# Kernel tuning notes

Measured on AMD Instinct MI355X. Metric: run time of the kernel, lower is better.

The kernel has to match this reference:

```python
import jax, jax.numpy as jnp
import numpy as np

B, T, D, H, DFF = 2, 2048, 1024, 16, 4096
K = D // H  # head size = 64
EPS = 1e-5


def _layernorm(x, g, b):
    mu = jnp.mean(x, axis=-1, keepdims=True)
    var = jnp.mean(jnp.square(x - mu), axis=-1, keepdims=True)
    return (x - mu) * jax.lax.rsqrt(var + EPS) * g + b


def setup_inputs() -> dict:
    key = jax.random.key(0)
    ks = jax.random.split(key, 12)
    s_attn = 1.0 / np.sqrt(D)
    s_ff1 = 1.0 / np.sqrt(D)
    s_ff2 = 1.0 / np.sqrt(DFF)
    return {
        "x": jax.random.normal(ks[0], (B, T, D), jnp.float32),
        # per-head q/k/v projections, stacked: [H, D, K] (each head's Linear has no bias)
        "Wq": jax.random.normal(ks[1], (H, D, K), jnp.float32) * s_attn,
        "Wk": jax.random.normal(ks[2], (H, D, K), jnp.float32) * s_attn,
        "Wv": jax.random.normal(ks[3], (H, D, K), jnp.float32) * s_attn,
        "Wo": jax.random.normal(ks[4], (D, D), jnp.float32) * s_attn,
        "bo": jax.random.normal(ks[5], (D,), jnp.float32) * 0.01,
        "W1": jax.random.normal(ks[6], (D, DFF), jnp.float32) * s_ff1,
        "b1": jax.random.normal(ks[7], (DFF,), jnp.float32) * 0.01,
        "W2": jax.random.normal(ks[8], (DFF, D), jnp.float32) * s_ff2,
        "b2": jax.random.normal(ks[9], (D,), jnp.float32) * 0.01,
        "g1": jnp.ones((D,), jnp.float32),
        "be1": jnp.zeros((D,), jnp.float32),
        "g2": jnp.ones((D,), jnp.float32),
        "be2": jnp.zeros((D,), jnp.float32),
    }


def reference(x, Wq, Wk, Wv, Wo, bo, W1, b1, W2, b2, g1, be1, g2, be2):
    b, t, d = x.shape
    h = _layernorm(x, g1, be1)
    # multi-head attention (per-head linear projections, fused via einsum)
    q = jnp.einsum('btd,hdk->bhtk', h, Wq)
    k = jnp.einsum('btd,hdk->bhtk', h, Wk)
    v = jnp.einsum('btd,hdk->bhtk', h, Wv)
    scores = jnp.einsum('bhtk,bhsk->bhts', q, k) * (K ** -0.5)
    causal = jnp.tril(jnp.ones((t, t), bool))
    scores = jnp.where(causal, scores, -jnp.inf)
    attn = jax.nn.softmax(scores, axis=-1)
    o = jnp.einsum('bhts,bhsk->bhtk', attn, v)
    o = o.transpose(0, 2, 1, 3).reshape(b, t, d)  # concat heads
    x = x + o @ Wo + bo
    # feed-forward (exact GELU, as torch default)
    h2 = _layernorm(x, g2, be2)
    ff = jax.nn.gelu(h2 @ W1 + b1, approximate=False) @ W2 + b2
    return x + ff
```

## Files before the change

kernel.cpp:

```cpp
#include <hip/hip_runtime.h>
#include <hip/hip_bf16.h>


#define BT   4096
#define DIM  1024
#define DFF  4096
#define TSEQ 2048
#define NHEAD 16
#define HDIM 64
#define QKV_LD 3072

typedef __attribute__((ext_vector_type(8))) short  bf16x8;
typedef __attribute__((ext_vector_type(4))) float  floatx4;

__device__ __forceinline__ void async_copy16(const __hip_bfloat16* g, __hip_bfloat16* l) {
    __builtin_amdgcn_global_load_lds(
        (const __attribute__((address_space(1))) void*)g,
        (__attribute__((address_space(3))) void*)l, 16, 0, 0);
}

__device__ __forceinline__ floatx4 mfma_bf16(bf16x8 a, bf16x8 b, floatx4 c) {
    return __builtin_amdgcn_mfma_f32_16x16x32_bf16(a, b, c, 0, 0, 0);
}

__device__ __forceinline__ void ln_body(const float* __restrict__ x,
                                        const float* __restrict__ g,
                                        const float* __restrict__ be,
                                        __hip_bfloat16* __restrict__ out,
                                        int row, float* red) {
    const int t = threadIdx.x;
    const float4 v = ((const float4*)(x + (size_t)row * DIM))[t];
    float s  = v.x + v.y + v.z + v.w;
    float ss = v.x * v.x + v.y * v.y + v.z * v.z + v.w * v.w;
    for (int d = 1; d < 64; d <<= 1) { s += __shfl_xor(s, d); ss += __shfl_xor(ss, d); }
    const int w = t >> 6;
    if ((t & 63) == 0) { red[w] = s; red[w + 4] = ss; }
    __syncthreads();
    s  = red[0] + red[1] + red[2] + red[3];
    ss = red[4] + red[5] + red[6] + red[7];
    const float mu = s * (1.0f / DIM);
    const float rstd = rsqrtf(ss * (1.0f / DIM) - mu * mu + 1e-5f);
    const float4 gv = ((const float4*)g)[t];
    const float4 bv = ((const float4*)be)[t];
    __hip_bfloat16* o = out + (size_t)row * DIM + t * 4;
    o[0] = __float2bfloat16((v.x - mu) * rstd * gv.x + bv.x);
    o[1] = __float2bfloat16((v.y - mu) * rstd * gv.y + bv.y);
    o[2] = __float2bfloat16((v.z - mu) * rstd * gv.z + bv.z);
    o[3] = __float2bfloat16((v.w - mu) * rstd * gv.w + bv.w);
}

__global__ __launch_bounds__(256) void ln_kernel(const float* __restrict__ x,
                                                 const float* __restrict__ g,
                                                 const float* __restrict__ be,
                                                 __hip_bfloat16* __restrict__ out) {
    __shared__ float red[8];
    ln_body(x, g, be, out, blockIdx.x, red);
}

__device__ __forceinline__ void tc_body(const float* __restrict__ src, int src_ld,
                                        __hip_bfloat16* __restrict__ dst, int dst_ld,
                                        int bx, int by, float* tile ) {
    const int r0 = bx * 64, c0 = by * 64;
    const int tr = threadIdx.x >> 6;
    const int tc = threadIdx.x & 63;
    for (int i = 0; i < 16; ++i) {
        const int r = i * 4 + tr;
        tile[r * 65 + tc] = src[(size_t)(r0 + r) * src_ld + c0 + tc];
    }
    __syncthreads();
    for (int i = 0; i < 16; ++i) {
        const int c = i * 4 + tr;
        dst[(size_t)(c0 + c) * dst_ld + r0 + tc] = __float2bfloat16(tile[tc * 65 + c]);
    }
}

__global__ __launch_bounds__(256) void prep_kernel(const float* __restrict__ x,
                                                   const float* __restrict__ g1,
                                                   const float* __restrict__ be1,
                                                   const float* __restrict__ Wq,
                                                   const float* __restrict__ Wk,
                                                   const float* __restrict__ Wv,
                                                   const float* __restrict__ Wo,
                                                   const float* __restrict__ W1,
                                                   const float* __restrict__ W2,
                                                   __hip_bfloat16* __restrict__ h1,
                                                   __hip_bfloat16* __restrict__ WqkvT,
                                                   __hip_bfloat16* __restrict__ WoT,
                                                   __hip_bfloat16* __restrict__ W1T,
                                                   __hip_bfloat16* __restrict__ W2T) {
    __shared__ __align__(16) float smemf[64 * 65];
    const int id = blockIdx.x;
    if (id < 4096) {
        ln_body(x, g1, be1, h1, id, smemf);
    } else if (id < 4096 + 768) {
        const int i = id - 4096;
        const int bx = i & 15, hz = i >> 4;
        const int proj = hz >> 4, h = hz & 15;
        const float* W = (proj == 0 ? Wq : (proj == 1 ? Wk : Wv)) + (size_t)h * DIM * HDIM;
        const int r0 = bx * 64;
        const int tr = threadIdx.x >> 6, tc = threadIdx.x & 63;
        for (int i2 = 0; i2 < 16; ++i2) {
            const int r = i2 * 4 + tr;
            smemf[r * 65 + tc] = W[(size_t)(r0 + r) * HDIM + tc];
        }
        __syncthreads();
        for (int i2 = 0; i2 < 16; ++i2) {
            const int k = i2 * 4 + tr;
            WqkvT[(size_t)(proj * 1024 + h * 64 + k) * DIM + r0 + tc] =
                __float2bfloat16(smemf[tc * 65 + k]);
        }
    } else if (id < 4096 + 768 + 256) {
        const int i = id - (4096 + 768);
        tc_body(Wo, 1024, WoT, 1024, i & 15, i >> 4, smemf);
    } else if (id < 4096 + 768 + 256 + 1024) {
        const int i = id - (4096 + 768 + 256);
        tc_body(W1, 4096, W1T, 1024, i & 15, i >> 4, smemf);
    } else {
        const int i = id - (4096 + 768 + 256 + 1024);
        tc_body(W2, 1024, W2T, 4096, i & 63, i >> 6, smemf);
    }
}

__global__ __launch_bounds__(256) void transpose_v(const __hip_bfloat16* __restrict__ qkv,
                                                   __hip_bfloat16* __restrict__ vt) {
    __shared__ __align__(16) __hip_bfloat16 tile[64 * 72];
    const int t = threadIdx.x;
    const int bh = blockIdx.y;
    const int b = bh >> 4, h = bh & 15;
    const int t0 = blockIdx.x * 64;
    const __hip_bfloat16* src = qkv + (size_t)b * TSEQ * QKV_LD + 2048 + h * HDIM;
    const int lo = t >> 3, k8 = t & 7;
    for (int i = 0; i < 2; ++i) {
        const int rr = i * 32 + lo;
        const bf16x8 v = *(const bf16x8*)(src + (size_t)(t0 + rr) * QKV_LD + k8 * 8);
        const int cb = k8 ^ ((rr >> 3) & 7);
        *(bf16x8*)(tile + rr * 72 + cb * 8) = v;
    }
    __syncthreads();
    for (int i = 0; i < 2; ++i) {
        const int dd = i * 32 + lo;
        const int c0 = dd >> 3, cl = dd & 7;
        bf16x8 o;
        for (int jj = 0; jj < 8; ++jj) {
            const int key = k8 * 8 + jj;
            o[jj] = *(const short*)(tile + key * 72 + (c0 ^ ((key >> 3) & 7)) * 8 + cl);
        }
        *(bf16x8*)(vt + ((size_t)bh * HDIM + dd) * TSEQ + t0 + k8 * 8) = o;
    }
}

template <int EPI>
__global__ __launch_bounds__(256) void gemm_bt(const __hip_bfloat16* __restrict__ A,
                                               const __hip_bfloat16* __restrict__ Bt,
                                               __hip_bfloat16* __restrict__ outb,
                                               const float* __restrict__ bias,
                                               int M, int N, int K) {
    __shared__ __align__(16) __hip_bfloat16 As[4][128 * 32];
    __shared__ __align__(16) __hip_bfloat16 Bs[4][128 * 32];
    const int t = threadIdx.x;
    const int w = t >> 6, l = t & 63;
    const int quad = l >> 4, tl = l & 15;
    const int wr = w >> 1, wc = w & 1;
    const int m0 = blockIdx.y * 128, n0 = blockIdx.x * 128;

    floatx4 acc[4][4] = {};
    const int rowA = t >> 2;
    const int c8 = (t & 3) << 3;

    for (int k0 = 0; k0 < K; k0 += 128) {
        __syncthreads();
        for (int sub = 0; sub < 4; ++sub) {
            const int kk = k0 + sub * 32;
            const __hip_bfloat16* gA = A + (size_t)(m0 + rowA) * K + kk + c8;
            const __hip_bfloat16* gB = Bt + (size_t)(n0 + rowA) * K + kk + c8;
            async_copy16(gA,                  As[sub] + w * 512);
            async_copy16(gA + (size_t)64 * K, As[sub] + 2048 + w * 512);
            async_copy16(gB,                  Bs[sub] + w * 512);
            async_copy16(gB + (size_t)64 * K, Bs[sub] + 2048 + w * 512);
        }
        __syncthreads();

        for (int ks = 0; ks < 4; ++ks) {
            bf16x8 af[4], bfr[4];
            const int aRow = wr * 64 + tl;
            const int bRow = wc * 64 + tl;
            for (int mi = 0; mi < 4; ++mi)
                af[mi] = *(const bf16x8*)(As[ks] + (aRow + mi * 16) * 32 + quad * 8);
            for (int ni = 0; ni < 4; ++ni)
                bfr[ni] = *(const bf16x8*)(Bs[ks] + (bRow + ni * 16) * 32 + quad * 8);
            for (int mi = 0; mi < 4; ++mi)
                for (int ni = 0; ni < 4; ++ni)
                    acc[mi][ni] = mfma_bf16(af[mi], bfr[ni], acc[mi][ni]);
        }
    }

    const int rowBase = m0 + wr * 64 + quad * 4;
    const int colBase = n0 + wc * 64 + tl;
    for (int mi = 0; mi < 4; ++mi) {
        for (int ni = 0; ni < 4; ++ni) {
            const int c = colBase + ni * 16;
            for (int j = 0; j < 4; ++j) {
                const int r = rowBase + mi * 16 + j;
                const size_t idx = (size_t)r * N + c;
                float v = acc[mi][ni][j];
                if (EPI == 1) {
                    v += bias[c];
                    v = 0.5f * v * (1.0f + erff(v * 0.70710678118654752f));
                }
                outb[idx] = __float2bfloat16(v);
            }
        }
    }
}

__global__ __launch_bounds__(256) void gemm_bt_k128(const __hip_bfloat16* __restrict__ A,
                                                    const __hip_bfloat16* __restrict__ Bt,
                                                    float* __restrict__ outf,
                                                    const float* __restrict__ bias,
                                                    const float* __restrict__ resid,
                                                    int M, int N, int K) {
    __shared__ __align__(16) __hip_bfloat16 As[128 * 128];
    __shared__ __align__(16) __hip_bfloat16 Bs[64 * 128];
    const int t = threadIdx.x;
    const int w = t >> 6, l = t & 63;
    const int quad = l >> 4, tl = l & 15;
    const int id = blockIdx.x;
    const int xcd = id & 7, jb = id >> 3;
    const int n0 = (jb & 15) * 64;
    const int m0 = ((jb >> 4) * 8 + xcd) * 128;

    floatx4 acc[2][4] = {};
    const int srow = t >> 4;
    const int scg  = t & 15;

    for (int k0 = 0; k0 < K; k0 += 128) {
        __syncthreads();
        for (int p = 0; p < 8; ++p) {
            const int row = p * 16 + srow;
            async_copy16(A + (size_t)(m0 + row) * K + k0 + ((scg ^ (row & 7)) << 3),
                         As + p * 2048 + w * 512);
        }
        for (int p = 0; p < 4; ++p) {
            const int row = p * 16 + srow;
            async_copy16(Bt + (size_t)(n0 + row) * K + k0 + ((scg ^ (row & 7)) << 3),
                         Bs + p * 2048 + w * 512);
        }
        __syncthreads();

        for (int ks = 0; ks < 4; ++ks) {
            bf16x8 af[2], bfr[4];
            for (int mi = 0; mi < 2; ++mi) {
                const int r = w * 32 + mi * 16 + tl;
                af[mi] = *(const bf16x8*)(As + r * 128 + (((ks * 4 + quad) ^ (r & 7)) << 3));
            }
            for (int ni = 0; ni < 4; ++ni) {
                const int r = ni * 16 + tl;
                bfr[ni] = *(const bf16x8*)(Bs + r * 128 + (((ks * 4 + quad) ^ (r & 7)) << 3));
            }
            for (int mi = 0; mi < 2; ++mi)
                for (int ni = 0; ni < 4; ++ni)
                    acc[mi][ni] = mfma_bf16(af[mi], bfr[ni], acc[mi][ni]);
        }
    }

    const int rowBase = m0 + w * 32 + quad * 4;
    const int colBase = n0 + tl;
    for (int mi = 0; mi < 2; ++mi) {
        for (int ni = 0; ni < 4; ++ni) {
            const int c = colBase + ni * 16;
            for (int j = 0; j < 4; ++j) {
                const int r = rowBase + mi * 16 + j;
                const size_t idx = (size_t)r * N + c;
                outf[idx] = resid[idx] + acc[mi][ni][j] + bias[c];
            }
        }
    }
}

#define KS_LD 72
#define VT_LD 72
#define PL_LD 72
__global__ __launch_bounds__(256) void attn_kernel(const __hip_bfloat16* __restrict__ qkv,
                                                   const __hip_bfloat16* __restrict__ vt,
                                                   __hip_bfloat16* __restrict__ out) {
    __shared__ __align__(16) __hip_bfloat16 Ks[64 * KS_LD];
    __shared__ __align__(16) __hip_bfloat16 Vts[64 * VT_LD];
    __shared__ __align__(16) __hip_bfloat16 Pl[4][16 * PL_LD];
    const int t = threadIdx.x;
    const int w = t >> 6, l = t & 63;
    const int quad = l >> 4, tl = l & 15;
    const int id = blockIdx.x;
    const int bh = ((id & 7) << 2) | ((id >> 3) & 3);
    const int pq = id >> 5;
    const int b = bh >> 4, h = bh & 15;
    const __hip_bfloat16* Qp  = qkv + (size_t)b * TSEQ * QKV_LD + h * HDIM;
    const __hip_bfloat16* Kp  = Qp + 1024;
    const __hip_bfloat16* Vtp = vt + (size_t)bh * HDIM * TSEQ;
    __hip_bfloat16* P = Pl[w];
    const float cscale = 0.125f * 1.4426950408889634f;
    const int srow = t >> 3, sk8 = t & 7;

    for (int half = 0; half < 2; ++half) {
        const int qb = half ? (31 - pq) : pq;
        const int qw = qb * 64 + w * 16;
        const int nb = qb + 1;

        const __hip_bfloat16* qrow = Qp + (size_t)(qw + tl) * QKV_LD + quad * 8;
        const bf16x8 qf0 = *(const bf16x8*)qrow;
        const bf16x8 qf1 = *(const bf16x8*)(qrow + 32);
        floatx4 oacc[4] = {};
        float l_i[4] = {0.0f, 0.0f, 0.0f, 0.0f};
        const int myrow = quad * 4;

        for (int it = 0; it < nb; ++it) {
            const int s0 = it * 64;
            __syncthreads();
            for (int i = 0; i < 2; ++i) {
                const int rr = i * 32 + srow;
                const bf16x8 kv = *(const bf16x8*)(Kp  + (size_t)(s0 + rr) * QKV_LD + sk8 * 8);
                const bf16x8 vv = *(const bf16x8*)(Vtp + (size_t)rr * TSEQ + s0 + sk8 * 8);
                *(bf16x8*)(Ks  + rr * KS_LD + sk8 * 8) = kv;
                *(bf16x8*)(Vts + rr * VT_LD + sk8 * 8) = vv;
            }
            __syncthreads();

            floatx4 sc[4];
            for (int ni = 0; ni < 4; ++ni) {
                const __hip_bfloat16* kr = Ks + (ni * 16 + tl) * KS_LD + quad * 8;
                floatx4 z = {0.0f, 0.0f, 0.0f, 0.0f};
                z = mfma_bf16(qf0, *(const bf16x8*)kr, z);
                sc[ni] = mfma_bf16(qf1, *(const bf16x8*)(kr + 32), z);
            }

            const bool lastB = (it == nb - 1);
            for (int ni = 0; ni < 4; ++ni) {
                const int keyrel = ni * 16 + tl - w * 16;
                for (int j = 0; j < 4; ++j) {
                    float pv = exp2f(sc[ni][j] * cscale);
                    if (lastB && keyrel > myrow + j) pv = 0.0f;
                    l_i[j] += pv;
                    P[(myrow + j) * PL_LD + ni * 16 + tl] = __float2bfloat16(pv);
                }
            }
            __builtin_amdgcn_wave_barrier();

            for (int kc = 0; kc < 2; ++kc) {
                const bf16x8 pf = *(const bf16x8*)(P + tl * PL_LD + kc * 32 + quad * 8);
                for (int ni = 0; ni < 4; ++ni) {
                    const bf16x8 vf = *(const bf16x8*)(Vts + (ni * 16 + tl) * VT_LD
                                                       + kc * 32 + quad * 8);
                    oacc[ni] = mfma_bf16(pf, vf, oacc[ni]);
                }
            }
        }

        for (int d = 1; d < 16; d <<= 1) {
            float r0 = __shfl_xor(l_i[0], d), r1 = __shfl_xor(l_i[1], d);
            float r2 = __shfl_xor(l_i[2], d), r3 = __shfl_xor(l_i[3], d);
            l_i[0] += r0; l_i[1] += r1; l_i[2] += r2; l_i[3] += r3;
        }
        for (int j = 0; j < 4; ++j) {
            const float inv = 1.0f / l_i[j];
            const int rg = qw + quad * 4 + j;
            __hip_bfloat16* orow = out + ((size_t)b * TSEQ + rg) * DIM + h * HDIM;
            for (int ni = 0; ni < 4; ++ni)
                orow[ni * 16 + tl] = __float2bfloat16(oacc[ni][j] * inv);
        }
    }
}

extern "C" void kernel_launch(void* const* d_in, const int* in_sizes, int n_in,
                              void* d_out, int out_size, void* d_ws, size_t ws_size,
                              hipStream_t stream) {
    const float* x   = (const float*)d_in[0];
    const float* Wq  = (const float*)d_in[1];
    const float* Wk  = (const float*)d_in[2];
    const float* Wv  = (const float*)d_in[3];
    const float* Wo  = (const float*)d_in[4];
    const float* bo  = (const float*)d_in[5];
    const float* W1  = (const float*)d_in[6];
    const float* b1  = (const float*)d_in[7];
    const float* W2  = (const float*)d_in[8];
    const float* b2  = (const float*)d_in[9];
    const float* g1  = (const float*)d_in[10];
    const float* be1 = (const float*)d_in[11];
    const float* g2  = (const float*)d_in[12];
    const float* be2 = (const float*)d_in[13];
    float* out = (float*)d_out;

    size_t off = 0;
    char* wsb = (char*)d_ws;
    auto carve = [&](size_t bytes) {
        void* p = wsb + off;
        off += (bytes + 255) & ~(size_t)255;
        return p;
    };
    __hip_bfloat16* WqkvT = (__hip_bfloat16*)carve((size_t)3072 * 1024 * 2);
    __hip_bfloat16* WoT   = (__hip_bfloat16*)carve((size_t)1024 * 1024 * 2);
    __hip_bfloat16* W1T   = (__hip_bfloat16*)carve((size_t)4096 * 1024 * 2);
    __hip_bfloat16* W2T   = (__hip_bfloat16*)carve((size_t)1024 * 4096 * 2);
    __hip_bfloat16* h1    = (__hip_bfloat16*)carve((size_t)BT * DIM * 2);
    __hip_bfloat16* qkv   = (__hip_bfloat16*)carve((size_t)BT * QKV_LD * 2);
    __hip_bfloat16* vtb   = (__hip_bfloat16*)carve((size_t)BT * DIM * 2);
    __hip_bfloat16* att   = (__hip_bfloat16*)carve((size_t)BT * DIM * 2);
    float*          x2    = (float*)carve((size_t)BT * DIM * 4);
    __hip_bfloat16* h2    = (__hip_bfloat16*)carve((size_t)BT * DIM * 2);
    __hip_bfloat16* ff1   = (__hip_bfloat16*)carve((size_t)BT * DFF * 2);

    prep_kernel<<<7168, 256, 0, stream>>>(x, g1, be1, Wq, Wk, Wv, Wo, W1, W2,
                                          h1, WqkvT, WoT, W1T, W2T);
    gemm_bt<0><<<dim3(24, 32), 256, 0, stream>>>(h1, WqkvT, qkv, nullptr, BT, QKV_LD, DIM);
    transpose_v<<<dim3(32, 32), 256, 0, stream>>>(qkv, vtb);
    attn_kernel<<<512, 256, 0, stream>>>(qkv, vtb, att);
    gemm_bt_k128<<<512, 256, 0, stream>>>(att, WoT, x2, bo, x, BT, DIM, DIM);
    ln_kernel<<<BT, 256, 0, stream>>>(x2, g2, be2, h2);
    gemm_bt<1><<<dim3(32, 32), 256, 0, stream>>>(h2, W1T, ff1, b1, BT, DFF, DIM);
    gemm_bt_k128<<<512, 256, 0, stream>>>(ff1, W2T, out, b2, x2, BT, DIM, DFF);
}
```

Baseline: 357.3 us.

## Fuse V transpose into QKV GEMM epilogue and double-buffer K/V tiles in attention

The QKV GEMM epilogue now writes the V columns directly in transposed [b,h,d,t] layout with packed 4-element stores. This removes the separate transpose_v kernel and its extra read and write of V. Q/K are stored in a narrower 2048-wide buffer. The attention kernel double-buffers its K and V^T shared-memory tiles, prefetching the next block into registers while computing on the current one, which uses one barrier per iteration instead of two. The trade-off is more LDS and registers in attention, and strided 8-byte global stores in the GEMM epilogue.

```diff
diff --git a/kernel.cpp b/kernel.cpp
--- a/kernel.cpp
+++ b/kernel.cpp
@@ -8,10 +8,11 @@
 #define TSEQ 2048
 #define NHEAD 16
 #define HDIM 64
-#define QKV_LD 3072
+#define QK_LD 2048
 
 typedef __attribute__((ext_vector_type(8))) short  bf16x8;
 typedef __attribute__((ext_vector_type(4))) float  floatx4;
+struct alignas(8) bf4 { __hip_bfloat16 x[4]; };
 
 __device__ __forceinline__ void async_copy16(const __hip_bfloat16* g, __hip_bfloat16* l) {
     __builtin_amdgcn_global_load_lds(
@@ -121,38 +122,11 @@
     }
 }
 
-__global__ __launch_bounds__(256) void transpose_v(const __hip_bfloat16* __restrict__ qkv,
-                                                   __hip_bfloat16* __restrict__ vt) {
-    __shared__ __align__(16) __hip_bfloat16 tile[64 * 72];
-    const int t = threadIdx.x;
-    const int bh = blockIdx.y;
-    const int b = bh >> 4, h = bh & 15;
-    const int t0 = blockIdx.x * 64;
-    const __hip_bfloat16* src = qkv + (size_t)b * TSEQ * QKV_LD + 2048 + h * HDIM;
-    const int lo = t >> 3, k8 = t & 7;
-    for (int i = 0; i < 2; ++i) {
-        const int rr = i * 32 + lo;
-        const bf16x8 v = *(const bf16x8*)(src + (size_t)(t0 + rr) * QKV_LD + k8 * 8);
-        const int cb = k8 ^ ((rr >> 3) & 7);
-        *(bf16x8*)(tile + rr * 72 + cb * 8) = v;
-    }
-    __syncthreads();
-    for (int i = 0; i < 2; ++i) {
-        const int dd = i * 32 + lo;
-        const int c0 = dd >> 3, cl = dd & 7;
-        bf16x8 o;
-        for (int jj = 0; jj < 8; ++jj) {
-            const int key = k8 * 8 + jj;
-            o[jj] = *(const short*)(tile + key * 72 + (c0 ^ ((key >> 3) & 7)) * 8 + cl);
-        }
-        *(bf16x8*)(vt + ((size_t)bh * HDIM + dd) * TSEQ + t0 + k8 * 8) = o;
-    }
-}
-
 template <int EPI>
 __global__ __launch_bounds__(256) void gemm_bt(const __hip_bfloat16* __restrict__ A,
                                                const __hip_bfloat16* __restrict__ Bt,
                                                __hip_bfloat16* __restrict__ outb,
+                                               __hip_bfloat16* __restrict__ vt,
                                                const float* __restrict__ bias,
                                                int M, int N, int K) {
     __shared__ __align__(16) __hip_bfloat16 As[4][128 * 32];
@@ -196,18 +170,33 @@
 
     const int rowBase = m0 + wr * 64 + quad * 4;
     const int colBase = n0 + wc * 64 + tl;
-    for (int mi = 0; mi < 4; ++mi) {
-        for (int ni = 0; ni < 4; ++ni) {
-            const int c = colBase + ni * 16;
-            for (int j = 0; j < 4; ++j) {
-                const int r = rowBase + mi * 16 + j;
-                const size_t idx = (size_t)r * N + c;
-                float v = acc[mi][ni][j];
-                if (EPI == 1) {
-                    v += bias[c];
-                    v = 0.5f * v * (1.0f + erff(v * 0.70710678118654752f));
+    if (EPI == 0 && n0 >= 2048) {
+        for (int mi = 0; mi < 4; ++mi) {
+            const int rb = rowBase + mi * 16;
+            const int bb = rb >> 11, trow = rb & 2047;
+            for (int ni = 0; ni < 4; ++ni) {
+                const int c = colBase + ni * 16;
+                const int hh = (c - 2048) >> 6, dd = (c - 2048) & 63;
+                bf4 pk;
+                for (int j = 0; j < 4; ++j) pk.x[j] = __float2bfloat16(acc[mi][ni][j]);
+                *(bf4*)(vt + (((size_t)(bb * 16 + hh)) * 64 + dd) * TSEQ + trow) = pk;
+            }
+        }
+    } else {
+        for (int mi = 0; mi < 4; ++mi) {
+            for (int ni = 0; ni < 4; ++ni) {
+                const int c = colBase + ni * 16;
+                for (int j = 0; j < 4; ++j) {
+                    const int r = rowBase + mi * 16 + j;
+                    float v = acc[mi][ni][j];
+                    if (EPI == 1) {
+                        v += bias[c];
+                        v = 0.5f * v * (1.0f + erff(v * 0.70710678118654752f));
+                        outb[(size_t)r * N + c] = __float2bfloat16(v);
+                    } else {
+                        outb[(size_t)r * QK_LD + c] = __float2bfloat16(v);
+                    }
                 }
-                outb[idx] = __float2bfloat16(v);
             }
         }
     }
@@ -280,11 +269,11 @@
 #define KS_LD 72
 #define VT_LD 72
 #define PL_LD 72
-__global__ __launch_bounds__(256) void attn_kernel(const __hip_bfloat16* __restrict__ qkv,
+__global__ __launch_bounds__(256) void attn_kernel(const __hip_bfloat16* __restrict__ qk,
                                                    const __hip_bfloat16* __restrict__ vt,
                                                    __hip_bfloat16* __restrict__ out) {
-    __shared__ __align__(16) __hip_bfloat16 Ks[64 * KS_LD];
-    __shared__ __align__(16) __hip_bfloat16 Vts[64 * VT_LD];
+    __shared__ __align__(16) __hip_bfloat16 Ks[2][64 * KS_LD];
+    __shared__ __align__(16) __hip_bfloat16 Vts[2][64 * VT_LD];
     __shared__ __align__(16) __hip_bfloat16 Pl[4][16 * PL_LD];
     const int t = threadIdx.x;
     const int w = t >> 6, l = t & 63;
@@ -293,7 +282,7 @@
     const int bh = ((id & 7) << 2) | ((id >> 3) & 3);
     const int pq = id >> 5;
     const int b = bh >> 4, h = bh & 15;
-    const __hip_bfloat16* Qp  = qkv + (size_t)b * TSEQ * QKV_LD + h * HDIM;
+    const __hip_bfloat16* Qp  = qk + (size_t)b * TSEQ * QK_LD + h * HDIM;
     const __hip_bfloat16* Kp  = Qp + 1024;
     const __hip_bfloat16* Vtp = vt + (size_t)bh * HDIM * TSEQ;
     __hip_bfloat16* P = Pl[w];
@@ -305,28 +294,39 @@
         const int qw = qb * 64 + w * 16;
         const int nb = qb + 1;
 
-        const __hip_bfloat16* qrow = Qp + (size_t)(qw + tl) * QKV_LD + quad * 8;
+        const __hip_bfloat16* qrow = Qp + (size_t)(qw + tl) * QK_LD + quad * 8;
         const bf16x8 qf0 = *(const bf16x8*)qrow;
         const bf16x8 qf1 = *(const bf16x8*)(qrow + 32);
         floatx4 oacc[4] = {};
         float l_i[4] = {0.0f, 0.0f, 0.0f, 0.0f};
         const int myrow = quad * 4;
 
+        __syncthreads();
+        for (int i = 0; i < 2; ++i) {
+            const int rr = i * 32 + srow;
+            *(bf16x8*)(Ks[0]  + rr * KS_LD + sk8 * 8) =
+                *(const bf16x8*)(Kp + (size_t)rr * QK_LD + sk8 * 8);
+            *(bf16x8*)(Vts[0] + rr * VT_LD + sk8 * 8) =
+                *(const bf16x8*)(Vtp + (size_t)rr * TSEQ + sk8 * 8);
+        }
+        __syncthreads();
+
         for (int it = 0; it < nb; ++it) {
-            const int s0 = it * 64;
-            __syncthreads();
-            for (int i = 0; i < 2; ++i) {
-                const int rr = i * 32 + srow;
-                const bf16x8 kv = *(const bf16x8*)(Kp  + (size_t)(s0 + rr) * QKV_LD + sk8 * 8);
-                const bf16x8 vv = *(const bf16x8*)(Vtp + (size_t)rr * TSEQ + s0 + sk8 * 8);
-                *(bf16x8*)(Ks  + rr * KS_LD + sk8 * 8) = kv;
-                *(bf16x8*)(Vts + rr * VT_LD + sk8 * 8) = vv;
-            }
-            __syncthreads();
+            const int cb = it & 1;
+            const bool pf = (it + 1 < nb);
+            bf16x8 krg[2], vrg[2];
+            if (pf) {
+                const int s0n = (it + 1) * 64;
+                for (int i = 0; i < 2; ++i) {
+                    const int rr = i * 32 + srow;
+                    krg[i] = *(const bf16x8*)(Kp + (size_t)(s0n + rr) * QK_LD + sk8 * 8);
+                    vrg[i] = *(const bf16x8*)(Vtp + (size_t)rr * TSEQ + s0n + sk8 * 8);
+                }
+            }
 
             floatx4 sc[4];
             for (int ni = 0; ni < 4; ++ni) {
-                const __hip_bfloat16* kr = Ks + (ni * 16 + tl) * KS_LD + quad * 8;
+                const __hip_bfloat16* kr = Ks[cb] + (ni * 16 + tl) * KS_LD + quad * 8;
                 floatx4 z = {0.0f, 0.0f, 0.0f, 0.0f};
                 z = mfma_bf16(qf0, *(const bf16x8*)kr, z);
                 sc[ni] = mfma_bf16(qf1, *(const bf16x8*)(kr + 32), z);
@@ -345,13 +345,22 @@
             __builtin_amdgcn_wave_barrier();
 
             for (int kc = 0; kc < 2; ++kc) {
-                const bf16x8 pf = *(const bf16x8*)(P + tl * PL_LD + kc * 32 + quad * 8);
+                const bf16x8 pfr = *(const bf16x8*)(P + tl * PL_LD + kc * 32 + quad * 8);
                 for (int ni = 0; ni < 4; ++ni) {
-                    const bf16x8 vf = *(const bf16x8*)(Vts + (ni * 16 + tl) * VT_LD
+                    const bf16x8 vf = *(const bf16x8*)(Vts[cb] + (ni * 16 + tl) * VT_LD
                                                        + kc * 32 + quad * 8);
-                    oacc[ni] = mfma_bf16(pf, vf, oacc[ni]);
+                    oacc[ni] = mfma_bf16(pfr, vf, oacc[ni]);
                 }
             }
+
+            if (pf) {
+                for (int i = 0; i < 2; ++i) {
+                    const int rr = i * 32 + srow;
+                    *(bf16x8*)(Ks[cb ^ 1]  + rr * KS_LD + sk8 * 8) = krg[i];
+                    *(bf16x8*)(Vts[cb ^ 1] + rr * VT_LD + sk8 * 8) = vrg[i];
+                }
+            }
+            __syncthreads();
         }
 
         for (int d = 1; d < 16; d <<= 1) {
@@ -400,7 +409,7 @@
     __hip_bfloat16* W1T   = (__hip_bfloat16*)carve((size_t)4096 * 1024 * 2);
     __hip_bfloat16* W2T   = (__hip_bfloat16*)carve((size_t)1024 * 4096 * 2);
     __hip_bfloat16* h1    = (__hip_bfloat16*)carve((size_t)BT * DIM * 2);
-    __hip_bfloat16* qkv   = (__hip_bfloat16*)carve((size_t)BT * QKV_LD * 2);
+    __hip_bfloat16* qkb   = (__hip_bfloat16*)carve((size_t)BT * QK_LD * 2);
     __hip_bfloat16* vtb   = (__hip_bfloat16*)carve((size_t)BT * DIM * 2);
     __hip_bfloat16* att   = (__hip_bfloat16*)carve((size_t)BT * DIM * 2);
     float*          x2    = (float*)carve((size_t)BT * DIM * 4);
@@ -409,11 +418,12 @@
 
     prep_kernel<<<7168, 256, 0, stream>>>(x, g1, be1, Wq, Wk, Wv, Wo, W1, W2,
                                           h1, WqkvT, WoT, W1T, W2T);
-    gemm_bt<0><<<dim3(24, 32), 256, 0, stream>>>(h1, WqkvT, qkv, nullptr, BT, QKV_LD, DIM);
-    transpose_v<<<dim3(32, 32), 256, 0, stream>>>(qkv, vtb);
-    attn_kernel<<<512, 256, 0, stream>>>(qkv, vtb, att);
+    gemm_bt<0><<<dim3(24, 32), 256, 0, stream>>>(h1, WqkvT, qkb, vtb, nullptr,
+                                                 BT, 3072, DIM);
+    attn_kernel<<<512, 256, 0, stream>>>(qkb, vtb, att);
     gemm_bt_k128<<<512, 256, 0, stream>>>(att, WoT, x2, bo, x, BT, DIM, DIM);
     ln_kernel<<<BT, 256, 0, stream>>>(x2, g2, be2, h2);
-    gemm_bt<1><<<dim3(32, 32), 256, 0, stream>>>(h2, W1T, ff1, b1, BT, DFF, DIM);
+    gemm_bt<1><<<dim3(32, 32), 256, 0, stream>>>(h2, W1T, ff1, nullptr, b1,
+                                                 BT, DFF, DIM);
     gemm_bt_k128<<<512, 256, 0, stream>>>(ff1, W2T, out, b2, x2, BT, DIM, DFF);
 }
```

Result: faster. 340.8 us (-4.6%).
